# Kernel optimization log

Hardware: AMD Instinct MI355X
Metric: run time of the kernel (lower is better)

## Reference

```python
import jax, jax.numpy as jnp
import numpy as np

B, T, R = 128, 20, 49           # batch, caption length, num regions (7x7)
V, E, H, FD, A = 10000, 512, 512, 512, 256  # vocab, embed, hidden, feature, attn dims


def setup_inputs() -> dict:
    key = jax.random.key(0)
    ks = jax.random.split(key, 16)
    s = 0.02
    return {
        "features": jax.random.normal(ks[0], (B, R, FD), dtype=jnp.float32),
        "captions": jax.random.randint(ks[1], (B, T), 0, V),
        "emb": jax.random.normal(ks[2], (V, E), dtype=jnp.float32) * s,
        "W_h": jax.random.normal(ks[3], (A, H), dtype=jnp.float32) * s,
        "b_h": jnp.zeros((A,), jnp.float32),
        "W_f": jax.random.normal(ks[4], (A, FD), dtype=jnp.float32) * s,
        "b_f": jnp.zeros((A,), jnp.float32),
        "v_w": jax.random.normal(ks[5], (A,), dtype=jnp.float32) * s,
        "v_b": jnp.zeros((), jnp.float32),
        "W_ih": jax.random.normal(ks[6], (4 * H, E + FD), dtype=jnp.float32) * s,
        "W_hh": jax.random.normal(ks[7], (4 * H, H), dtype=jnp.float32) * s,
        "b_ih": jnp.zeros((4 * H,), jnp.float32),
        "b_hh": jnp.zeros((4 * H,), jnp.float32),
        "fc_W": jax.random.normal(ks[8], (V, H), dtype=jnp.float32) * s,
        "fc_b": jnp.zeros((V,), jnp.float32),
    }


def reference(features, captions, emb, W_h, b_h, W_f, b_f, v_w, v_b,
              W_ih, W_hh, b_ih, b_hh, fc_W, fc_b):
    Bn = features.shape[0]
    Hd = W_hh.shape[1]
    # features are constant across timesteps -> project once (same math as per-step W_f(features))
    f_proj = jnp.einsum('brf,af->bra', features, W_f) + b_f  # (B,R,A)
    embeds = emb[captions[:, :-1]]                            # (B,T-1,E)
    xs = jnp.swapaxes(embeds, 0, 1)                           # (T-1,B,E)
    bias = b_ih + b_hh

    def step(carry, x_t):
        hx, cx = carry
        # Bahdanau attention
        h = hx @ W_h.T + b_h                                  # (B,A)
        scores = jnp.tanh(h[:, None, :] + f_proj) @ v_w + v_b  # (B,R)
        alpha = jax.nn.softmax(scores, axis=1)
        context = jnp.einsum('br,brf->bf', alpha, features)   # (B,FD)
        # LSTMCell (PyTorch gate order: i,f,g,o)
        lstm_in = jnp.concatenate([x_t, context], axis=1)     # (B,E+FD)
        gates = lstm_in @ W_ih.T + hx @ W_hh.T + bias         # (B,4H)
        i, f, g, o = jnp.split(gates, 4, axis=1)
        cx = jax.nn.sigmoid(f) * cx + jax.nn.sigmoid(i) * jnp.tanh(g)
        hx = jax.nn.sigmoid(o) * jnp.tanh(cx)
        logit = hx @ fc_W.T + fc_b                            # (B,V)
        return (hx, cx), logit

    init = (jnp.zeros((Bn, Hd), features.dtype), jnp.zeros((Bn, Hd), features.dtype))
    _, logits = jax.lax.scan(step, init, xs)                  # (T-1,B,V)
    return jnp.swapaxes(logits, 0, 1)                         # (B,T-1,V)
```

## Files before the change

kernel.cpp:

```cpp
#include <hip/hip_runtime.h>
#include <hip/hip_bf16.h>
#include <math.h>

#define NB 128
#define NT 20
#define NS 19
#define NR 49
#define NV 10000
#define NE 512
#define NH 512
#define NFD 512
#define NA 256
#define NG 2048
#define NK2 1024

typedef __bf16 bf16_t;
typedef bf16_t bf16x8 __attribute__((ext_vector_type(8)));
typedef bf16_t bf16x4 __attribute__((ext_vector_type(4)));
typedef float f32x4 __attribute__((ext_vector_type(4)));

__device__ __forceinline__ float sigm(float x) { return 1.f / (1.f + expf(-x)); }

__device__ __forceinline__ void cvt8(bf16_t* d, const float* s) {
    float4 a = *(const float4*)s;
    float4 b = *(const float4*)(s + 4);
    bf16x8 v;
    v[0] = (bf16_t)a.x; v[1] = (bf16_t)a.y; v[2] = (bf16_t)a.z; v[3] = (bf16_t)a.w;
    v[4] = (bf16_t)b.x; v[5] = (bf16_t)b.y; v[6] = (bf16_t)b.z; v[7] = (bf16_t)b.w;
    *(bf16x8*)d = v;
}

__global__ __launch_bounds__(256) void k_prep(
    const float* __restrict__ fc_W, const float* __restrict__ W_ih,
    const float* __restrict__ W_hh, const float* __restrict__ W_h,
    const float* __restrict__ W_f, const float* __restrict__ features,
    const float* __restrict__ emb, const int* __restrict__ captions,
    const float* __restrict__ b_ih, const float* __restrict__ b_hh,
    const float* __restrict__ b_f, const float* __restrict__ b_h,
    bf16_t* __restrict__ fcWb, bf16_t* __restrict__ Wcat2,
    bf16_t* __restrict__ Wxg, bf16_t* __restrict__ W_hb,
    bf16_t* __restrict__ Wfb, bf16_t* __restrict__ featb,
    bf16_t* __restrict__ linx, float* __restrict__ bias,
    float* __restrict__ bfh, float* __restrict__ hx, float* __restrict__ cx,
    unsigned* __restrict__ cnt)
{
    int g = blockIdx.x * 256 + threadIdx.x;
    if (g < 640000) { int idx = g * 8; cvt8(fcWb + idx, fc_W + idx); return; }
    g -= 640000;
    if (g < 262144) {
        int idx = g * 8;
        int row = idx >> 10, col = idx & 1023;
        int orig = (row & 3) * NH + (row >> 2);
        const float* src = (col < 512) ? (W_ih + (size_t)orig * 1024 + 512 + col)
                                       : (W_hh + (size_t)orig * 512 + (col - 512));
        cvt8(Wcat2 + idx, src);
        return;
    }
    g -= 262144;
    if (g < 131072) {
        int idx = g * 8;
        int row = idx >> 9, col = idx & 511;
        int orig = (row & 3) * NH + (row >> 2);
        cvt8(Wxg + idx, W_ih + (size_t)orig * 1024 + col);
        return;
    }
    g -= 131072;
    if (g < 16384) { int idx = g * 8; cvt8(W_hb + idx, W_h + idx); return; }
    g -= 16384;
    if (g < 16384) { int idx = g * 8; cvt8(Wfb + idx, W_f + idx); return; }
    g -= 16384;
    if (g < 401408) { int idx = g * 8; cvt8(featb + idx, features + idx); return; }
    g -= 401408;
    if (g < 155648) {
        int idx = g * 8;
        int row = idx >> 9, col = idx & 511;
        int t = row >> 7, b = row & 127;
        int cap = captions[b * NT + t];
        cvt8(linx + idx, emb + (size_t)cap * NE + col);
        return;
    }
    g -= 155648;
    if (g < 256) {
        int n0 = g * 8;
        #pragma unroll
        for (int i = 0; i < 8; ++i) {
            int n = n0 + i, h = n >> 2, gg = n & 3;
            int orig = gg * NH + h;
            bias[n] = b_ih[orig] + b_hh[orig];
        }
        return;
    }
    g -= 256;
    if (g < 32) {
        int n0 = g * 8;
        #pragma unroll
        for (int i = 0; i < 8; ++i) bfh[n0 + i] = b_f[n0 + i] + b_h[n0 + i];
        return;
    }
    g -= 32;
    float4 z = make_float4(0.f, 0.f, 0.f, 0.f);
    if (g < 8192) { *(float4*)(hx + g * 8) = z; *(float4*)(hx + g * 8 + 4) = z; return; }
    g -= 8192;
    if (g < 8192) { *(float4*)(cx + g * 8) = z; *(float4*)(cx + g * 8 + 4) = z; return; }
    g -= 8192;
    if (g < 16) {
        #pragma unroll
        for (int i = 0; i < 8; ++i) cnt[g * 8 + i] = 0u;
    }
}

__global__ __launch_bounds__(256) void gemm_bf16_nt(
    const bf16_t* __restrict__ Am, const bf16_t* __restrict__ Bm,
    const float* __restrict__ bias, float* __restrict__ Cf,
    bf16_t* __restrict__ Cb, int M, int N, int K, int ldc)
{
    __shared__ uint4 AsU[512];
    __shared__ uint4 BsU[512];
    int tid = threadIdx.x;
    int m0 = blockIdx.x * 64, n0 = blockIdx.y * 64;
    int nk = K >> 6;

    int rowS = tid >> 3, slotS = tid & 7;
    int wr0 = rowS * 8 + (slotS ^ (rowS & 7));
    int rowS2 = rowS + 32;
    int wr1 = rowS2 * 8 + (slotS ^ (rowS2 & 7));

    const uint4* pA = (const uint4*)(Am + (size_t)(m0 + rowS) * K) + slotS;
    size_t aStep = (size_t)4 * K;
    int nrow0 = n0 + rowS, nrow1 = n0 + rowS2;
    bool bv0 = nrow0 < N, bv1 = nrow1 < N;
    const uint4* pB0 = (const uint4*)(Bm + (size_t)nrow0 * K) + slotS;
    const uint4* pB1 = (const uint4*)(Bm + (size_t)nrow1 * K) + slotS;
    uint4 zz = make_uint4(0, 0, 0, 0);

    int w = tid >> 6, lane = tid & 63;
    int wm = w >> 1, wn = w & 1;
    int lr = lane & 15, lg = lane >> 4;
    int ra[2][2], rb[2][2];
    #pragma unroll
    for (int i = 0; i < 2; ++i)
        #pragma unroll
        for (int kk = 0; kk < 2; ++kk) {
            int rA = wm * 32 + i * 16 + lr;
            int rB = wn * 32 + i * 16 + lr;
            int s = kk * 4 + lg;
            ra[i][kk] = rA * 8 + (s ^ (rA & 7));
            rb[i][kk] = rB * 8 + (s ^ (rB & 7));
        }

    f32x4 acc00 = {}, acc01 = {}, acc10 = {}, acc11 = {};
    uint4 a0 = pA[0], a1 = pA[aStep];
    uint4 b0 = bv0 ? pB0[0] : zz;
    uint4 b1 = bv1 ? pB1[0] : zz;
    pA += 8; pB0 += 8; pB1 += 8;

    #pragma unroll 1
    for (int kt = 0; kt < nk; ++kt) {
        __syncthreads();
        AsU[wr0] = a0; AsU[wr1] = a1;
        BsU[wr0] = b0; BsU[wr1] = b1;
        if (kt + 1 < nk) {
            a0 = pA[0]; a1 = pA[aStep];
            b0 = bv0 ? pB0[0] : zz;
            b1 = bv1 ? pB1[0] : zz;
            pA += 8; pB0 += 8; pB1 += 8;
        }
        __syncthreads();
        const bf16x8* Af = (const bf16x8*)AsU;
        const bf16x8* Bf = (const bf16x8*)BsU;
        #pragma unroll
        for (int kk = 0; kk < 2; ++kk) {
            bf16x8 fa0 = Af[ra[0][kk]], fa1 = Af[ra[1][kk]];
            bf16x8 fb0 = Bf[rb[0][kk]], fb1 = Bf[rb[1][kk]];
            acc00 = __builtin_amdgcn_mfma_f32_16x16x32_bf16(fa0, fb0, acc00, 0, 0, 0);
            acc01 = __builtin_amdgcn_mfma_f32_16x16x32_bf16(fa0, fb1, acc01, 0, 0, 0);
            acc10 = __builtin_amdgcn_mfma_f32_16x16x32_bf16(fa1, fb0, acc10, 0, 0, 0);
            acc11 = __builtin_amdgcn_mfma_f32_16x16x32_bf16(fa1, fb1, acc11, 0, 0, 0);
        }
    }

    f32x4 av[2][2] = {{acc00, acc01}, {acc10, acc11}};
    #pragma unroll
    for (int i = 0; i < 2; ++i) {
        int mbase = m0 + wm * 32 + i * 16 + lg * 4;
        #pragma unroll
        for (int j = 0; j < 2; ++j) {
            int n = n0 + wn * 32 + j * 16 + lr;
            if (n < N) {
                float bz = bias ? bias[n] : 0.f;
                #pragma unroll
                for (int r = 0; r < 4; ++r) {
                    float v = av[i][j][r] + bz;
                    if (Cb) Cb[(size_t)(mbase + r) * ldc + n] = (bf16_t)v;
                    else    Cf[(size_t)(mbase + r) * ldc + n] = v;
                }
            }
        }
    }
}

__global__ __launch_bounds__(512) void k_attn(
    const float* __restrict__ hx, const bf16_t* __restrict__ W_hb,
    const bf16_t* __restrict__ fprojb, const float* __restrict__ v_w,
    const bf16_t* __restrict__ featb, bf16_t* __restrict__ lin)
{
    int b = blockIdx.x;
    int tid = threadIdx.x;
    int w = tid >> 6, lane = tid & 63;
    __shared__ float hxs[NH];
    __shared__ float part[2][NA];
    __shared__ float salpha[64];

    hxs[tid] = hx[b * NH + tid];
    __syncthreads();

    {
        int a = tid & 255, q = tid >> 8;
        const bf16x8* wrow = (const bf16x8*)(W_hb + (size_t)a * NH + q * 256);
        const float* hq = hxs + q * 256;
        float p = 0.f;
        #pragma unroll
        for (int c = 0; c < 32; ++c) {
            bf16x8 wv = wrow[c];
            int k = c * 8;
            p += hq[k+0]*(float)wv[0] + hq[k+1]*(float)wv[1]
               + hq[k+2]*(float)wv[2] + hq[k+3]*(float)wv[3]
               + hq[k+4]*(float)wv[4] + hq[k+5]*(float)wv[5]
               + hq[k+6]*(float)wv[6] + hq[k+7]*(float)wv[7];
        }
        part[q][a] = p;
    }
    __syncthreads();

    {
        for (int r = w; r < NR; r += 8) {
            const bf16_t* fp = fprojb + ((size_t)b * NR + r) * NA;
            float s = 0.f;
            #pragma unroll
            for (int j = 0; j < 4; ++j) {
                int aa = lane + 64 * j;
                float hv = part[0][aa] + part[1][aa];
                s += tanhf(hv + (float)fp[aa]) * v_w[aa];
            }
            #pragma unroll
            for (int off = 32; off; off >>= 1) s += __shfl_xor(s, off);
            if (lane == 0) salpha[r] = s;
        }
    }
    __syncthreads();

    if (tid < 64) {
        float v = (tid < NR) ? salpha[tid] : -INFINITY;
        float m = v;
        #pragma unroll
        for (int off = 32; off; off >>= 1) m = fmaxf(m, __shfl_xor(m, off));
        float e = (tid < NR) ? expf(v - m) : 0.f;
        float ssum = e;
        #pragma unroll
        for (int off = 32; off; off >>= 1) ssum += __shfl_xor(ssum, off);
        if (tid < NR) salpha[tid] = e / ssum;
    }
    __syncthreads();

    {
        bf16_t* lrow = lin + (size_t)b * NK2;
        float c = 0.f;
        #pragma unroll 7
        for (int r = 0; r < NR; ++r)
            c += salpha[r] * (float)featb[((size_t)b * NR + r) * NFD + tid];
        lrow[tid] = (bf16_t)c;
        lrow[NFD + tid] = (bf16_t)hxs[tid];
    }
}

__global__ __launch_bounds__(512) void k_fused(
    bf16_t* lin,
    const bf16_t* __restrict__ Wcat2, const bf16_t* __restrict__ pre_x,
    const float* __restrict__ bias, float* hx,
    float* __restrict__ cx, bf16_t* __restrict__ hxAll,
    const bf16_t* __restrict__ W_hb, const bf16_t* __restrict__ fprojb,
    const float* __restrict__ v_w, const bf16_t* __restrict__ featb,
    unsigned* cnt, int t, int last)
{
    __shared__ __align__(16) char smem[20736];
    uint4* AsU = (uint4*)smem;
    uint4* BsU = AsU + 256;

    int tid = threadIdx.x;
    int xcd = blockIdx.x & 7, loc = blockIdx.x >> 3;
    int jg = xcd * 4 + (loc & 3);
    int ig = loc >> 2;
    int m0 = ig * 32, n0 = jg * 64;

    int rowS = tid >> 3, slotS = tid & 7;
    int wrB = rowS * 8 + (slotS ^ (rowS & 7));
    bool hasA = rowS < 32;
    int arow = hasA ? (m0 + rowS) : m0;

    const uint4* pB = (const uint4*)(Wcat2 + (size_t)(n0 + rowS) * NK2) + slotS;
    const uint4* pA = (const uint4*)(lin + (size_t)arow * NK2) + slotS;

    int w = tid >> 6, lane = tid & 63;
    int wm = w & 1, wn = w >> 1;
    int lr = lane & 15, lg = lane >> 4;
    int raI[2], rbI[2];
    #pragma unroll
    for (int kk = 0; kk < 2; ++kk) {
        int s = kk * 4 + lg;
        int rA = wm * 16 + lr;
        int rB = wn * 16 + lr;
        raI[kk] = rA * 8 + (s ^ (rA & 7));
        rbI[kk] = rB * 8 + (s ^ (rB & 7));
    }

    f32x4 acc = {};
    uint4 aR = {}, bR = pB[0];
    if (hasA) aR = pA[0];
    pB += 8; pA += 8;

    #pragma unroll 1
    for (int kt = 0; kt < NK2 / 64; ++kt) {
        __syncthreads();
        BsU[wrB] = bR;
        if (hasA) AsU[wrB] = aR;
        if (kt + 1 < NK2 / 64) {
            bR = pB[0]; pB += 8;
            if (hasA) { aR = pA[0]; pA += 8; }
        }
        __syncthreads();
        const bf16x8* Af = (const bf16x8*)AsU;
        const bf16x8* Bf = (const bf16x8*)BsU;
        #pragma unroll
        for (int kk = 0; kk < 2; ++kk) {
            bf16x8 fa = Af[raI[kk]];
            bf16x8 fb = Bf[rbI[kk]];
            acc = __builtin_amdgcn_mfma_f32_16x16x32_bf16(fa, fb, acc, 0, 0, 0);
        }
    }

    __syncthreads();
    float* Ct = (float*)smem;
    {
        int crow = wm * 16 + lg * 4;
        int ccol = wn * 16 + lr;
        #pragma unroll
        for (int r = 0; r < 4; ++r)
            Ct[(crow + r) * 65 + ccol] = acc[r];
    }
    __syncthreads();

    {
        int hloc = tid & 15, m = tid >> 4;
        int bb2 = m0 + m;
        int h = (n0 >> 2) + hloc;
        const float* crow = Ct + m * 65 + hloc * 4;
        const float* brow = bias + n0 + hloc * 4;
        const bf16_t* prow = pre_x + ((size_t)t * NB + bb2) * NG + n0 + hloc * 4;
        float gi = crow[0] + brow[0] + (float)prow[0];
        float gf = crow[1] + brow[1] + (float)prow[1];
        float gg = crow[2] + brow[2] + (float)prow[2];
        float go = crow[3] + brow[3] + (float)prow[3];
        size_t idx = (size_t)bb2 * NH + h;
        float c = sigm(gf) * cx[idx] + sigm(gi) * tanhf(gg);
        float hn = sigm(go) * tanhf(c);
        cx[idx] = c;
        __hip_atomic_store(hx + idx, hn, __ATOMIC_RELAXED,
                           __HIP_MEMORY_SCOPE_AGENT);
        hxAll[((size_t)t * NB + bb2) * NH + h] = (bf16_t)hn;
    }
    if (last) return;

    __syncthreads();
    unsigned* flag = cnt + t * 4 + ig;
    if (tid == 0) {
        __hip_atomic_fetch_add(flag, 1u, __ATOMIC_RELAXED,
                               __HIP_MEMORY_SCOPE_AGENT);
        while (__hip_atomic_load(flag, __ATOMIC_RELAXED,
                                 __HIP_MEMORY_SCOPE_AGENT) < 32u)
            __builtin_amdgcn_s_sleep(2);
    }
    __syncthreads();

    int bb = m0 + jg;
    float* hxs  = (float*)smem;
    float* part = hxs + 512;
    float* salp = part + 512;
    float* ctxp = salp + 64;

    hxs[tid] = __hip_atomic_load(hx + (size_t)bb * NH + tid,
                                 __ATOMIC_RELAXED, __HIP_MEMORY_SCOPE_AGENT);
    __syncthreads();

    {
        int a = tid & 255, q = tid >> 8;
        const bf16x8* wrow = (const bf16x8*)(W_hb + (size_t)a * NH + q * 256);
        const float* hq = hxs + q * 256;
        float p = 0.f;
        #pragma unroll
        for (int c = 0; c < 32; ++c) {
            bf16x8 wv = wrow[c];
            int k = c * 8;
            p += hq[k+0]*(float)wv[0] + hq[k+1]*(float)wv[1]
               + hq[k+2]*(float)wv[2] + hq[k+3]*(float)wv[3]
               + hq[k+4]*(float)wv[4] + hq[k+5]*(float)wv[5]
               + hq[k+6]*(float)wv[6] + hq[k+7]*(float)wv[7];
        }
        part[q * 256 + a] = p;
    }
    __syncthreads();
    if (tid < 256) part[tid] += part[256 + tid];
    __syncthreads();

    {
        for (int r = w; r < NR; r += 8) {
            bf16x4 fp4 = *(const bf16x4*)(fprojb + ((size_t)bb * NR + r) * NA + lane * 4);
            float4 vw4 = *(const float4*)(v_w + lane * 4);
            const float* hb = part + lane * 4;
            float s = tanhf(hb[0] + (float)fp4[0]) * vw4.x
                    + tanhf(hb[1] + (float)fp4[1]) * vw4.y
                    + tanhf(hb[2] + (float)fp4[2]) * vw4.z
                    + tanhf(hb[3] + (float)fp4[3]) * vw4.w;
            #pragma unroll
            for (int off = 32; off; off >>= 1) s += __shfl_xor(s, off);
            if (lane == 0) salp[r] = s;
        }
    }
    __syncthreads();

    if (tid < 64) {
        float v = (tid < NR) ? salp[tid] : -INFINITY;
        float m = v;
        #pragma unroll
        for (int off = 32; off; off >>= 1) m = fmaxf(m, __shfl_xor(m, off));
        float e = (tid < NR) ? expf(v - m) : 0.f;
        float ssum = e;
        #pragma unroll
        for (int off = 32; off; off >>= 1) ssum += __shfl_xor(ssum, off);
        if (tid < NR) salp[tid] = e / ssum;
    }
    __syncthreads();

    {
        int ck = tid & 63, rg = tid >> 6;
        float c[8] = {};
        for (int r = rg; r < NR; r += 8) {
            bf16x8 v = *(const bf16x8*)(featb + ((size_t)bb * NR + r) * NFD + ck * 8);
            float al = salp[r];
            #pragma unroll
            for (int jj = 0; jj < 8; ++jj) c[jj] += al * (float)v[jj];
        }
        float* cp = ctxp + (rg * 64 + ck) * 8;
        #pragma unroll
        for (int jj = 0; jj < 8; ++jj) cp[jj] = c[jj];
    }
    __syncthreads();

    {
        float cc = 0.f;
        #pragma unroll
        for (int rg = 0; rg < 8; ++rg) cc += ctxp[rg * 512 + tid];
        bf16_t* lrow = lin + (size_t)bb * NK2;
        lrow[tid]       = (bf16_t)cc;
        lrow[512 + tid] = (bf16_t)hxs[tid];
    }
}

__global__ __launch_bounds__(256) void k_logits(
    const bf16_t* __restrict__ hxAll, const bf16_t* __restrict__ fcWb,
    const float* __restrict__ fc_b, float* __restrict__ out)
{
    __shared__ uint4 AsU[512];
    __shared__ uint4 BsU[512];
    int tid = threadIdx.x;
    int m0 = blockIdx.x * 64, n0 = blockIdx.y * 64;

    int rowS = tid >> 3, slotS = tid & 7;
    int wr0 = rowS * 8 + (slotS ^ (rowS & 7));
    int rowS2 = rowS + 32;
    int wr1 = rowS2 * 8 + (slotS ^ (rowS2 & 7));

    const uint4* pA = (const uint4*)(hxAll + (size_t)(m0 + rowS) * NH) + slotS;
    size_t aStep = (size_t)4 * NH;
    int nrow0 = n0 + rowS, nrow1 = n0 + rowS2;
    bool bv0 = nrow0 < NV, bv1 = nrow1 < NV;
    const uint4* pB0 = (const uint4*)(fcWb + (size_t)nrow0 * NH) + slotS;
    const uint4* pB1 = (const uint4*)(fcWb + (size_t)nrow1 * NH) + slotS;
    uint4 zz = make_uint4(0, 0, 0, 0);

    int w = tid >> 6, lane = tid & 63;
    int wm = w >> 1, wn = w & 1;
    int lr = lane & 15, lg = lane >> 4;
    int ra[2][2], rb[2][2];
    #pragma unroll
    for (int i = 0; i < 2; ++i)
        #pragma unroll
        for (int kk = 0; kk < 2; ++kk) {
            int rA = wm * 32 + i * 16 + lr;
            int rB = wn * 32 + i * 16 + lr;
            int s = kk * 4 + lg;
            ra[i][kk] = rA * 8 + (s ^ (rA & 7));
            rb[i][kk] = rB * 8 + (s ^ (rB & 7));
        }

    f32x4 acc00 = {}, acc01 = {}, acc10 = {}, acc11 = {};
    uint4 a0 = pA[0], a1 = pA[aStep];
    uint4 b0 = bv0 ? pB0[0] : zz;
    uint4 b1 = bv1 ? pB1[0] : zz;
    pA += 8; pB0 += 8; pB1 += 8;

    #pragma unroll 1
    for (int kt = 0; kt < NH / 64; ++kt) {
        __syncthreads();
        AsU[wr0] = a0; AsU[wr1] = a1;
        BsU[wr0] = b0; BsU[wr1] = b1;
        if (kt + 1 < NH / 64) {
            a0 = pA[0]; a1 = pA[aStep];
            b0 = bv0 ? pB0[0] : zz;
            b1 = bv1 ? pB1[0] : zz;
            pA += 8; pB0 += 8; pB1 += 8;
        }
        __syncthreads();
        const bf16x8* Af = (const bf16x8*)AsU;
        const bf16x8* Bf = (const bf16x8*)BsU;
        #pragma unroll
        for (int kk = 0; kk < 2; ++kk) {
            bf16x8 fa0 = Af[ra[0][kk]], fa1 = Af[ra[1][kk]];
            bf16x8 fb0 = Bf[rb[0][kk]], fb1 = Bf[rb[1][kk]];
            acc00 = __builtin_amdgcn_mfma_f32_16x16x32_bf16(fa0, fb0, acc00, 0, 0, 0);
            acc01 = __builtin_amdgcn_mfma_f32_16x16x32_bf16(fa0, fb1, acc01, 0, 0, 0);
            acc10 = __builtin_amdgcn_mfma_f32_16x16x32_bf16(fa1, fb0, acc10, 0, 0, 0);
            acc11 = __builtin_amdgcn_mfma_f32_16x16x32_bf16(fa1, fb1, acc11, 0, 0, 0);
        }
    }

    f32x4 av[2][2] = {{acc00, acc01}, {acc10, acc11}};
    #pragma unroll
    for (int i = 0; i < 2; ++i) {
        int mbase = m0 + wm * 32 + i * 16 + lg * 4;
        #pragma unroll
        for (int j = 0; j < 2; ++j) {
            int n = n0 + wn * 32 + j * 16 + lr;
            if (n < NV) {
                float bz = fc_b[n];
                #pragma unroll
                for (int r = 0; r < 4; ++r) {
                    int m = mbase + r;
                    int bb = m & 127, tt = m >> 7;
                    __builtin_nontemporal_store(
                        av[i][j][r] + bz,
                        out + ((size_t)bb * NS + tt) * NV + n);
                }
            }
        }
    }
}

extern "C" void kernel_launch(void* const* d_in, const int* in_sizes, int n_in,
                              void* d_out, int out_size, void* d_ws, size_t ws_size,
                              hipStream_t stream)
{
    const float* features = (const float*)d_in[0];
    const int*   captions = (const int*)d_in[1];
    const float* emb      = (const float*)d_in[2];
    const float* W_h      = (const float*)d_in[3];
    const float* b_h      = (const float*)d_in[4];
    const float* W_f      = (const float*)d_in[5];
    const float* b_f      = (const float*)d_in[6];
    const float* v_w      = (const float*)d_in[7];
    const float* W_ih     = (const float*)d_in[9];
    const float* W_hh     = (const float*)d_in[10];
    const float* b_ih     = (const float*)d_in[11];
    const float* b_hh     = (const float*)d_in[12];
    const float* fc_W     = (const float*)d_in[13];
    const float* fc_b     = (const float*)d_in[14];
    float* out = (float*)d_out;

    char* base = (char*)d_ws;
    bf16_t* fcWb   = (bf16_t*)base;  base += (size_t)NV * NH * 2;
    bf16_t* Wcat2  = (bf16_t*)base;  base += (size_t)NG * NK2 * 2;
    bf16_t* Wxg    = (bf16_t*)base;  base += (size_t)NG * NE * 2;
    bf16_t* W_hb   = (bf16_t*)base;  base += (size_t)NA * NH * 2;
    bf16_t* Wfb    = (bf16_t*)base;  base += (size_t)NA * NFD * 2;
    bf16_t* featb  = (bf16_t*)base;  base += (size_t)NB * NR * NFD * 2;
    bf16_t* linx   = (bf16_t*)base;  base += (size_t)NS * NB * NE * 2;
    bf16_t* pre_x  = (bf16_t*)base;  base += (size_t)NS * NB * NG * 2;
    bf16_t* lin    = (bf16_t*)base;  base += (size_t)NB * NK2 * 2;
    bf16_t* hxAll  = (bf16_t*)base;  base += (size_t)NS * NB * NH * 2;
    bf16_t* fprojb = (bf16_t*)base;  base += (size_t)NB * NR * NA * 2;
    float*  bias   = (float*)base;   base += (size_t)NG * 4;
    float*  bfh    = (float*)base;   base += (size_t)NA * 4;
    float*  hx     = (float*)base;   base += (size_t)NB * NH * 4;
    float*  cx     = (float*)base;   base += (size_t)NB * NH * 4;
    unsigned* cnt  = (unsigned*)base; base += 128 * 4;

    k_prep<<<dim3(6406), 256, 0, stream>>>(
        fc_W, W_ih, W_hh, W_h, W_f, features, emb, captions, b_ih, b_hh,
        b_f, b_h, fcWb, Wcat2, Wxg, W_hb, Wfb, featb, linx, bias, bfh,
        hx, cx, cnt);

    gemm_bf16_nt<<<dim3(98, 4), 256, 0, stream>>>(
        featb, Wfb, bfh, (float*)0, fprojb, NB * NR, NA, NFD, NA);

    gemm_bf16_nt<<<dim3(38, 32), 256, 0, stream>>>(
        linx, Wxg, (const float*)0, (float*)0, pre_x, NS * NB, NG, NE, NG);

    k_attn<<<dim3(NB), 512, 0, stream>>>(hx, W_hb, fprojb, v_w, featb, lin);

    for (int t = 0; t < NS; ++t) {
        k_fused<<<dim3(128), 512, 0, stream>>>(
            lin, Wcat2, pre_x, bias, hx, cx, hxAll,
            W_hb, fprojb, v_w, featb, cnt, t, (t == NS - 1) ? 1 : 0);
    }

    k_logits<<<dim3(38, 157), 256, 0, stream>>>(hxAll, fcWb, fc_b, out);
}
```

Measured before the change: 569.4 us.

## Replace per-timestep kernel launches with one persistent cooperative kernel

Folds the 19 per-step fused LSTM/attention launches into a single cooperative kernel that loops over timesteps inside the kernel. Blocks synchronise through global atomic counter barriers, two per step. The LSTM input buffer becomes per-timestep so that writing the next step's input cannot race with other blocks still reading the current one. This removes launch overhead and the kernel-boundary drain between steps, at the cost of an extra spin barrier per step and a larger workspace.

```diff
diff --git a/kernel.cpp b/kernel.cpp
--- a/kernel.cpp
+++ b/kernel.cpp
@@ -17,6 +17,7 @@
 typedef __bf16 bf16_t;
 typedef bf16_t bf16x8 __attribute__((ext_vector_type(8)));
 typedef bf16_t bf16x4 __attribute__((ext_vector_type(4)));
+typedef bf16_t bf16x2 __attribute__((ext_vector_type(2)));
 typedef float f32x4 __attribute__((ext_vector_type(4)));
 
 __device__ __forceinline__ float sigm(float x) { return 1.f / (1.f + expf(-x)); }
@@ -103,7 +104,7 @@
     g -= 8192;
     if (g < 8192) { *(float4*)(cx + g * 8) = z; *(float4*)(cx + g * 8 + 4) = z; return; }
     g -= 8192;
-    if (g < 16) {
+    if (g < 32) {
         #pragma unroll
         for (int i = 0; i < 8; ++i) cnt[g * 8 + i] = 0u;
     }
@@ -273,14 +274,14 @@
     }
 }
 
-__global__ __launch_bounds__(512) void k_fused(
-    bf16_t* lin,
+__global__ __launch_bounds__(512) void k_persist(
+    bf16_t* linS,
     const bf16_t* __restrict__ Wcat2, const bf16_t* __restrict__ pre_x,
     const float* __restrict__ bias, float* hx,
     float* __restrict__ cx, bf16_t* __restrict__ hxAll,
     const bf16_t* __restrict__ W_hb, const bf16_t* __restrict__ fprojb,
     const float* __restrict__ v_w, const bf16_t* __restrict__ featb,
-    unsigned* cnt, int t, int last)
+    unsigned* cnt)
 {
     __shared__ __align__(16) char smem[20736];
     uint4* AsU = (uint4*)smem;
@@ -297,8 +298,7 @@
     bool hasA = rowS < 32;
     int arow = hasA ? (m0 + rowS) : m0;
 
-    const uint4* pB = (const uint4*)(Wcat2 + (size_t)(n0 + rowS) * NK2) + slotS;
-    const uint4* pA = (const uint4*)(lin + (size_t)arow * NK2) + slotS;
+    const uint4* pBbase = (const uint4*)(Wcat2 + (size_t)(n0 + rowS) * NK2) + slotS;
 
     int w = tid >> 6, lane = tid & 63;
     int wm = w & 1, wn = w >> 1;
@@ -313,155 +313,187 @@
         rbI[kk] = rB * 8 + (s ^ (rB & 7));
     }
 
-    f32x4 acc = {};
-    uint4 aR = {}, bR = pB[0];
-    if (hasA) aR = pA[0];
-    pB += 8; pA += 8;
+    int bb = m0 + jg;
 
     #pragma unroll 1
-    for (int kt = 0; kt < NK2 / 64; ++kt) {
-        __syncthreads();
-        BsU[wrB] = bR;
-        if (hasA) AsU[wrB] = aR;
-        if (kt + 1 < NK2 / 64) {
-            bR = pB[0]; pB += 8;
-            if (hasA) { aR = pA[0]; pA += 8; }
-        }
-        __syncthreads();
-        const bf16x8* Af = (const bf16x8*)AsU;
-        const bf16x8* Bf = (const bf16x8*)BsU;
-        #pragma unroll
-        for (int kk = 0; kk < 2; ++kk) {
-            bf16x8 fa = Af[raI[kk]];
-            bf16x8 fb = Bf[rbI[kk]];
-            acc = __builtin_amdgcn_mfma_f32_16x16x32_bf16(fa, fb, acc, 0, 0, 0);
-        }
-    }
-
-    __syncthreads();
-    float* Ct = (float*)smem;
-    {
-        int crow = wm * 16 + lg * 4;
-        int ccol = wn * 16 + lr;
-        #pragma unroll
-        for (int r = 0; r < 4; ++r)
-            Ct[(crow + r) * 65 + ccol] = acc[r];
-    }
-    __syncthreads();
-
-    {
-        int hloc = tid & 15, m = tid >> 4;
-        int bb2 = m0 + m;
-        int h = (n0 >> 2) + hloc;
-        const float* crow = Ct + m * 65 + hloc * 4;
-        const float* brow = bias + n0 + hloc * 4;
-        const bf16_t* prow = pre_x + ((size_t)t * NB + bb2) * NG + n0 + hloc * 4;
-        float gi = crow[0] + brow[0] + (float)prow[0];
-        float gf = crow[1] + brow[1] + (float)prow[1];
-        float gg = crow[2] + brow[2] + (float)prow[2];
-        float go = crow[3] + brow[3] + (float)prow[3];
-        size_t idx = (size_t)bb2 * NH + h;
-        float c = sigm(gf) * cx[idx] + sigm(gi) * tanhf(gg);
-        float hn = sigm(go) * tanhf(c);
-        cx[idx] = c;
-        __hip_atomic_store(hx + idx, hn, __ATOMIC_RELAXED,
-                           __HIP_MEMORY_SCOPE_AGENT);
-        hxAll[((size_t)t * NB + bb2) * NH + h] = (bf16_t)hn;
-    }
-    if (last) return;
-
-    __syncthreads();
-    unsigned* flag = cnt + t * 4 + ig;
-    if (tid == 0) {
-        __hip_atomic_fetch_add(flag, 1u, __ATOMIC_RELAXED,
+    for (int t = 0; t < NS; ++t) {
+        const uint4* pA = (const uint4*)(linS + ((size_t)t * NB + arow) * NK2) + slotS;
+        const uint4* pB = pBbase;
+        f32x4 acc = {};
+        uint4 aR = {}, bR = pB[0];
+        if (hasA) aR = pA[0];
+        pB += 8; pA += 8;
+
+        #pragma unroll 1
+        for (int kt = 0; kt < NK2 / 64; ++kt) {
+            __syncthreads();
+            BsU[wrB] = bR;
+            if (hasA) AsU[wrB] = aR;
+            if (kt + 1 < NK2 / 64) {
+                bR = pB[0]; pB += 8;
+                if (hasA) { aR = pA[0]; pA += 8; }
+            }
+            __syncthreads();
+            const bf16x8* Af = (const bf16x8*)AsU;
+            const bf16x8* Bf = (const bf16x8*)BsU;
+            #pragma unroll
+            for (int kk = 0; kk < 2; ++kk) {
+                bf16x8 fa = Af[raI[kk]];
+                bf16x8 fb = Bf[rbI[kk]];
+                acc = __builtin_amdgcn_mfma_f32_16x16x32_bf16(fa, fb, acc, 0, 0, 0);
+            }
+        }
+
+        __syncthreads();
+        float* Ct = (float*)smem;
+        {
+            int crow = wm * 16 + lg * 4;
+            int ccol = wn * 16 + lr;
+            #pragma unroll
+            for (int r = 0; r < 4; ++r)
+                Ct[(crow + r) * 65 + ccol] = acc[r];
+        }
+        __syncthreads();
+
+        {
+            int hloc = tid & 15, m = tid >> 4;
+            int bb2 = m0 + m;
+            int h = (n0 >> 2) + hloc;
+            const float* crow = Ct + m * 65 + hloc * 4;
+            const float* brow = bias + n0 + hloc * 4;
+            const bf16_t* prow = pre_x + ((size_t)t * NB + bb2) * NG + n0 + hloc * 4;
+            float gi = crow[0] + brow[0] + (float)prow[0];
+            float gf = crow[1] + brow[1] + (float)prow[1];
+            float gg = crow[2] + brow[2] + (float)prow[2];
+            float go = crow[3] + brow[3] + (float)prow[3];
+            size_t idx = (size_t)bb2 * NH + h;
+            float c = sigm(gf) * cx[idx] + sigm(gi) * tanhf(gg);
+            float hn = sigm(go) * tanhf(c);
+            cx[idx] = c;
+            __hip_atomic_store(hx + idx, hn, __ATOMIC_RELAXED,
                                __HIP_MEMORY_SCOPE_AGENT);
-        while (__hip_atomic_load(flag, __ATOMIC_RELAXED,
-                                 __HIP_MEMORY_SCOPE_AGENT) < 32u)
-            __builtin_amdgcn_s_sleep(2);
-    }
-    __syncthreads();
-
-    int bb = m0 + jg;
-    float* hxs  = (float*)smem;
-    float* part = hxs + 512;
-    float* salp = part + 512;
-    float* ctxp = salp + 64;
-
-    hxs[tid] = __hip_atomic_load(hx + (size_t)bb * NH + tid,
-                                 __ATOMIC_RELAXED, __HIP_MEMORY_SCOPE_AGENT);
-    __syncthreads();
-
-    {
-        int a = tid & 255, q = tid >> 8;
-        const bf16x8* wrow = (const bf16x8*)(W_hb + (size_t)a * NH + q * 256);
-        const float* hq = hxs + q * 256;
-        float p = 0.f;
-        #pragma unroll
-        for (int c = 0; c < 32; ++c) {
-            bf16x8 wv = wrow[c];
-            int k = c * 8;
-            p += hq[k+0]*(float)wv[0] + hq[k+1]*(float)wv[1]
-               + hq[k+2]*(float)wv[2] + hq[k+3]*(float)wv[3]
-               + hq[k+4]*(float)wv[4] + hq[k+5]*(float)wv[5]
-               + hq[k+6]*(float)wv[6] + hq[k+7]*(float)wv[7];
-        }
-        part[q * 256 + a] = p;
-    }
-    __syncthreads();
-    if (tid < 256) part[tid] += part[256 + tid];
-    __syncthreads();
-
-    {
-        for (int r = w; r < NR; r += 8) {
-            bf16x4 fp4 = *(const bf16x4*)(fprojb + ((size_t)bb * NR + r) * NA + lane * 4);
-            float4 vw4 = *(const float4*)(v_w + lane * 4);
-            const float* hb = part + lane * 4;
-            float s = tanhf(hb[0] + (float)fp4[0]) * vw4.x
-                    + tanhf(hb[1] + (float)fp4[1]) * vw4.y
-                    + tanhf(hb[2] + (float)fp4[2]) * vw4.z
-                    + tanhf(hb[3] + (float)fp4[3]) * vw4.w;
-            #pragma unroll
-            for (int off = 32; off; off >>= 1) s += __shfl_xor(s, off);
-            if (lane == 0) salp[r] = s;
-        }
-    }
-    __syncthreads();
-
-    if (tid < 64) {
-        float v = (tid < NR) ? salp[tid] : -INFINITY;
-        float m = v;
-        #pragma unroll
-        for (int off = 32; off; off >>= 1) m = fmaxf(m, __shfl_xor(m, off));
-        float e = (tid < NR) ? expf(v - m) : 0.f;
-        float ssum = e;
-        #pragma unroll
-        for (int off = 32; off; off >>= 1) ssum += __shfl_xor(ssum, off);
-        if (tid < NR) salp[tid] = e / ssum;
-    }
-    __syncthreads();
-
-    {
-        int ck = tid & 63, rg = tid >> 6;
-        float c[8] = {};
-        for (int r = rg; r < NR; r += 8) {
-            bf16x8 v = *(const bf16x8*)(featb + ((size_t)bb * NR + r) * NFD + ck * 8);
-            float al = salp[r];
-            #pragma unroll
-            for (int jj = 0; jj < 8; ++jj) c[jj] += al * (float)v[jj];
-        }
-        float* cp = ctxp + (rg * 64 + ck) * 8;
-        #pragma unroll
-        for (int jj = 0; jj < 8; ++jj) cp[jj] = c[jj];
-    }
-    __syncthreads();
-
-    {
-        float cc = 0.f;
-        #pragma unroll
-        for (int rg = 0; rg < 8; ++rg) cc += ctxp[rg * 512 + tid];
-        bf16_t* lrow = lin + (size_t)bb * NK2;
-        lrow[tid]       = (bf16_t)cc;
-        lrow[512 + tid] = (bf16_t)hxs[tid];
+            hxAll[((size_t)t * NB + bb2) * NH + h] = (bf16_t)hn;
+        }
+        if (t == NS - 1) break;
+
+        __syncthreads();
+        {
+            unsigned* flag = cnt + t * 8 + ig;
+            if (tid == 0) {
+                __hip_atomic_fetch_add(flag, 1u, __ATOMIC_RELAXED,
+                                       __HIP_MEMORY_SCOPE_AGENT);
+                while (__hip_atomic_load(flag, __ATOMIC_RELAXED,
+                                         __HIP_MEMORY_SCOPE_AGENT) < 32u)
+                    __builtin_amdgcn_s_sleep(2);
+            }
+        }
+        __syncthreads();
+
+        float* hxs  = (float*)smem;
+        float* part = hxs + 512;
+        float* salp = part + 512;
+        float* ctxp = salp + 64;
+        float* ctxf = part;
+
+        hxs[tid] = __hip_atomic_load(hx + (size_t)bb * NH + tid,
+                                     __ATOMIC_RELAXED, __HIP_MEMORY_SCOPE_AGENT);
+        __syncthreads();
+
+        {
+            int a = tid & 255, q = tid >> 8;
+            const bf16x8* wrow = (const bf16x8*)(W_hb + (size_t)a * NH + q * 256);
+            const float* hq = hxs + q * 256;
+            float p = 0.f;
+            #pragma unroll
+            for (int c = 0; c < 32; ++c) {
+                bf16x8 wv = wrow[c];
+                int k = c * 8;
+                p += hq[k+0]*(float)wv[0] + hq[k+1]*(float)wv[1]
+                   + hq[k+2]*(float)wv[2] + hq[k+3]*(float)wv[3]
+                   + hq[k+4]*(float)wv[4] + hq[k+5]*(float)wv[5]
+                   + hq[k+6]*(float)wv[6] + hq[k+7]*(float)wv[7];
+            }
+            part[q * 256 + a] = p;
+        }
+        __syncthreads();
+        if (tid < 256) part[tid] += part[256 + tid];
+        __syncthreads();
+
+        {
+            for (int r = w; r < NR; r += 8) {
+                bf16x4 fp4 = *(const bf16x4*)(fprojb + ((size_t)bb * NR + r) * NA + lane * 4);
+                float4 vw4 = *(const float4*)(v_w + lane * 4);
+                const float* hb = part + lane * 4;
+                float s = tanhf(hb[0] + (float)fp4[0]) * vw4.x
+                        + tanhf(hb[1] + (float)fp4[1]) * vw4.y
+                        + tanhf(hb[2] + (float)fp4[2]) * vw4.z
+                        + tanhf(hb[3] + (float)fp4[3]) * vw4.w;
+                #pragma unroll
+                for (int off = 32; off; off >>= 1) s += __shfl_xor(s, off);
+                if (lane == 0) salp[r] = s;
+            }
+        }
+        __syncthreads();
+
+        if (tid < 64) {
+            float v = (tid < NR) ? salp[tid] : -INFINITY;
+            float m = v;
+            #pragma unroll
+            for (int off = 32; off; off >>= 1) m = fmaxf(m, __shfl_xor(m, off));
+            float e = (tid < NR) ? expf(v - m) : 0.f;
+            float ssum = e;
+            #pragma unroll
+            for (int off = 32; off; off >>= 1) ssum += __shfl_xor(ssum, off);
+            if (tid < NR) salp[tid] = e / ssum;
+        }
+        __syncthreads();
+
+        {
+            int ck = tid & 63, rg = tid >> 6;
+            float c[8] = {};
+            for (int r = rg; r < NR; r += 8) {
+                bf16x8 v = *(const bf16x8*)(featb + ((size_t)bb * NR + r) * NFD + ck * 8);
+                float al = salp[r];
+                #pragma unroll
+                for (int jj = 0; jj < 8; ++jj) c[jj] += al * (float)v[jj];
+            }
+            float* cp = ctxp + (rg * 64 + ck) * 8;
+            #pragma unroll
+            for (int jj = 0; jj < 8; ++jj) cp[jj] = c[jj];
+        }
+        __syncthreads();
+
+        {
+            float cc = 0.f;
+            #pragma unroll
+            for (int rg = 0; rg < 8; ++rg) cc += ctxp[rg * 512 + tid];
+            ctxf[tid] = cc;
+        }
+        __syncthreads();
+
+        {
+            unsigned* lrow = (unsigned*)(linS + ((size_t)(t + 1) * NB + bb) * NK2);
+            float lo, hi;
+            if (tid < 256) { lo = ctxf[2 * tid]; hi = ctxf[2 * tid + 1]; }
+            else           { lo = hxs[2 * tid - 512]; hi = hxs[2 * tid - 511]; }
+            bf16x2 v2;
+            v2[0] = (bf16_t)lo; v2[1] = (bf16_t)hi;
+            __hip_atomic_store(lrow + tid, __builtin_bit_cast(unsigned, v2),
+                               __ATOMIC_RELAXED, __HIP_MEMORY_SCOPE_AGENT);
+        }
+
+        __syncthreads();
+        {
+            unsigned* flag = cnt + t * 8 + 4 + ig;
+            if (tid == 0) {
+                __hip_atomic_fetch_add(flag, 1u, __ATOMIC_RELAXED,
+                                       __HIP_MEMORY_SCOPE_AGENT);
+                while (__hip_atomic_load(flag, __ATOMIC_RELAXED,
+                                         __HIP_MEMORY_SCOPE_AGENT) < 32u)
+                    __builtin_amdgcn_s_sleep(2);
+            }
+        }
+        __syncthreads();
     }
 }
 
@@ -584,14 +616,14 @@
     bf16_t* featb  = (bf16_t*)base;  base += (size_t)NB * NR * NFD * 2;
     bf16_t* linx   = (bf16_t*)base;  base += (size_t)NS * NB * NE * 2;
     bf16_t* pre_x  = (bf16_t*)base;  base += (size_t)NS * NB * NG * 2;
-    bf16_t* lin    = (bf16_t*)base;  base += (size_t)NB * NK2 * 2;
+    bf16_t* linS   = (bf16_t*)base;  base += (size_t)NT * NB * NK2 * 2;
     bf16_t* hxAll  = (bf16_t*)base;  base += (size_t)NS * NB * NH * 2;
     bf16_t* fprojb = (bf16_t*)base;  base += (size_t)NB * NR * NA * 2;
     float*  bias   = (float*)base;   base += (size_t)NG * 4;
     float*  bfh    = (float*)base;   base += (size_t)NA * 4;
     float*  hx     = (float*)base;   base += (size_t)NB * NH * 4;
     float*  cx     = (float*)base;   base += (size_t)NB * NH * 4;
-    unsigned* cnt  = (unsigned*)base; base += 128 * 4;
+    unsigned* cnt  = (unsigned*)base; base += 256 * 4;
 
     k_prep<<<dim3(6406), 256, 0, stream>>>(
         fc_W, W_ih, W_hh, W_h, W_f, features, emb, captions, b_ih, b_hh,
@@ -604,13 +636,14 @@
     gemm_bf16_nt<<<dim3(38, 32), 256, 0, stream>>>(
         linx, Wxg, (const float*)0, (float*)0, pre_x, NS * NB, NG, NE, NG);
 
-    k_attn<<<dim3(NB), 512, 0, stream>>>(hx, W_hb, fprojb, v_w, featb, lin);
-
-    for (int t = 0; t < NS; ++t) {
-        k_fused<<<dim3(128), 512, 0, stream>>>(
-            lin, Wcat2, pre_x, bias, hx, cx, hxAll,
-            W_hb, fprojb, v_w, featb, cnt, t, (t == NS - 1) ? 1 : 0);
-    }
+    k_attn<<<dim3(NB), 512, 0, stream>>>(hx, W_hb, fprojb, v_w, featb, linS);
+
+    void* kargs[] = {
+        (void*)&linS, (void*)&Wcat2, (void*)&pre_x, (void*)&bias,
+        (void*)&hx, (void*)&cx, (void*)&hxAll, (void*)&W_hb,
+        (void*)&fprojb, (void*)&v_w, (void*)&featb, (void*)&cnt };
+    hipLaunchCooperativeKernel((const void*)k_persist, dim3(128), dim3(512),
+                               kargs, 0, stream);
 
     k_logits<<<dim3(38, 157), 256, 0, stream>>>(hxAll, fcWb, fc_b, out);
 }
```

Result: slower. 947.7 us (+66.4%).

## Replace contended atomic counter barrier with per-block flags; swizzle logits grid by XCD

Applied to the files above, without the earlier changes.

The inter-block barrier in the fused step kernel used to have 32 blocks fetch-add one counter and spin on it. It now uses one flag word per block, and 32 threads each poll a separate flag, which removes atomic contention on a single cache line. The logits GEMM also moves to a 1D grid with an XCD-aware swizzle, so consecutive tiles on the same XCD share weight rows in L2. The cost is more flag memory, one slot per step, and more polling threads.

```diff
diff --git a/kernel.cpp b/kernel.cpp
--- a/kernel.cpp
+++ b/kernel.cpp
@@ -42,7 +42,7 @@
     bf16_t* __restrict__ Wfb, bf16_t* __restrict__ featb,
     bf16_t* __restrict__ linx, float* __restrict__ bias,
     float* __restrict__ bfh, float* __restrict__ hx, float* __restrict__ cx,
-    unsigned* __restrict__ cnt)
+    unsigned* __restrict__ flags)
 {
     int g = blockIdx.x * 256 + threadIdx.x;
     if (g < 640000) { int idx = g * 8; cvt8(fcWb + idx, fc_W + idx); return; }
@@ -103,9 +103,9 @@
     g -= 8192;
     if (g < 8192) { *(float4*)(cx + g * 8) = z; *(float4*)(cx + g * 8 + 4) = z; return; }
     g -= 8192;
-    if (g < 16) {
-        #pragma unroll
-        for (int i = 0; i < 8; ++i) cnt[g * 8 + i] = 0u;
+    if (g < 304) {
+        #pragma unroll
+        for (int i = 0; i < 8; ++i) flags[g * 8 + i] = 0u;
     }
 }
 
@@ -280,7 +280,7 @@
     float* __restrict__ cx, bf16_t* __restrict__ hxAll,
     const bf16_t* __restrict__ W_hb, const bf16_t* __restrict__ fprojb,
     const float* __restrict__ v_w, const bf16_t* __restrict__ featb,
-    unsigned* cnt, int t, int last)
+    unsigned* flags, int t, int last)
 {
     __shared__ __align__(16) char smem[20736];
     uint4* AsU = (uint4*)smem;
@@ -371,13 +371,16 @@
     if (last) return;
 
     __syncthreads();
-    unsigned* flag = cnt + t * 4 + ig;
-    if (tid == 0) {
-        __hip_atomic_fetch_add(flag, 1u, __ATOMIC_RELAXED,
+    {
+        unsigned* fl = flags + t * 128 + ig * 32;
+        if (tid == 0)
+            __hip_atomic_store(fl + jg, 1u, __ATOMIC_RELAXED,
                                __HIP_MEMORY_SCOPE_AGENT);
-        while (__hip_atomic_load(flag, __ATOMIC_RELAXED,
-                                 __HIP_MEMORY_SCOPE_AGENT) < 32u)
-            __builtin_amdgcn_s_sleep(2);
+        if (tid < 32) {
+            while (__hip_atomic_load(fl + tid, __ATOMIC_RELAXED,
+                                     __HIP_MEMORY_SCOPE_AGENT) == 0u)
+                __builtin_amdgcn_s_sleep(2);
+        }
     }
     __syncthreads();
 
@@ -469,10 +472,16 @@
     const bf16_t* __restrict__ hxAll, const bf16_t* __restrict__ fcWb,
     const float* __restrict__ fc_b, float* __restrict__ out)
 {
+    const int NWG = 38 * 157, Q = NWG / 8, RR = NWG % 8;
+    int bid = blockIdx.x;
+    int xcd = bid & 7, loc = bid >> 3;
+    int swz = (xcd < RR ? xcd * (Q + 1) : RR * (Q + 1) + (xcd - RR) * Q) + loc;
+    int m0 = (swz % 38) * 64;
+    int n0 = (swz / 38) * 64;
+
     __shared__ uint4 AsU[512];
     __shared__ uint4 BsU[512];
     int tid = threadIdx.x;
-    int m0 = blockIdx.x * 64, n0 = blockIdx.y * 64;
 
     int rowS = tid >> 3, slotS = tid & 7;
     int wr0 = rowS * 8 + (slotS ^ (rowS & 7));
@@ -591,12 +600,12 @@
     float*  bfh    = (float*)base;   base += (size_t)NA * 4;
     float*  hx     = (float*)base;   base += (size_t)NB * NH * 4;
     float*  cx     = (float*)base;   base += (size_t)NB * NH * 4;
-    unsigned* cnt  = (unsigned*)base; base += 128 * 4;
-
-    k_prep<<<dim3(6406), 256, 0, stream>>>(
+    unsigned* flags = (unsigned*)base; base += (size_t)NS * 128 * 4;
+
+    k_prep<<<dim3(6407), 256, 0, stream>>>(
         fc_W, W_ih, W_hh, W_h, W_f, features, emb, captions, b_ih, b_hh,
         b_f, b_h, fcWb, Wcat2, Wxg, W_hb, Wfb, featb, linx, bias, bfh,
-        hx, cx, cnt);
+        hx, cx, flags);
 
     gemm_bf16_nt<<<dim3(98, 4), 256, 0, stream>>>(
         featb, Wfb, bfh, (float*)0, fprojb, NB * NR, NA, NFD, NA);
@@ -609,8 +618,8 @@
     for (int t = 0; t < NS; ++t) {
         k_fused<<<dim3(128), 512, 0, stream>>>(
             lin, Wcat2, pre_x, bias, hx, cx, hxAll,
-            W_hb, fprojb, v_w, featb, cnt, t, (t == NS - 1) ? 1 : 0);
-    }
-
-    k_logits<<<dim3(38, 157), 256, 0, stream>>>(hxAll, fcWb, fc_b, out);
+            W_hb, fprojb, v_w, featb, flags, t, (t == NS - 1) ? 1 : 0);
+    }
+
+    k_logits<<<dim3(38 * 157), 256, 0, stream>>>(hxAll, fcWb, fc_b, out);
 }
```

Result: faster. 549.9 us (median of 2 runs) (-3.4%).
